# Optimization experiments

Measured on AMD Instinct MI355X. Metric: run time of the kernel, lower is better.

## Reference

```python
import jax, jax.numpy as jnp
import numpy as np

DIM = 256
HID = DIM // 8  # 32


def setup_inputs() -> dict:
    key = jax.random.key(0)
    ks = jax.random.split(key, 16)
    B, N, M, C = 4, 4096, 16, DIM
    q = jax.random.normal(ks[0], (B, N, C), dtype=jnp.float32)
    k = jax.random.normal(ks[1], (B, N, M, C), dtype=jnp.float32)
    pos = jax.random.normal(ks[2], (B, N, M, 4), dtype=jnp.float32)
    mask = jax.random.randint(ks[3], (B, N, M, 1), 0, 2, dtype=jnp.int32)
    s = 1.0 / np.sqrt(C)
    # weights stored [in, out]; apply as x @ W (+ b)
    Ws = jax.random.normal(ks[4], (C, C), dtype=jnp.float32) * s
    Wp1 = jax.random.normal(ks[5], (4, HID), dtype=jnp.float32) * 0.5
    bp1 = jnp.zeros((HID,), dtype=jnp.float32)
    Wp2 = jax.random.normal(ks[6], (HID, C), dtype=jnp.float32) * (1.0 / np.sqrt(HID))
    bp2 = jnp.zeros((C,), dtype=jnp.float32)
    Wa1 = jax.random.normal(ks[7], (C, HID), dtype=jnp.float32) * s
    ba1 = jnp.zeros((HID,), dtype=jnp.float32)
    Wa2 = jax.random.normal(ks[8], (HID, C), dtype=jnp.float32) * (1.0 / np.sqrt(HID))
    ba2 = jnp.zeros((C,), dtype=jnp.float32)
    Wo = jax.random.normal(ks[9], (C, C), dtype=jnp.float32) * s
    bo = jnp.zeros((C,), dtype=jnp.float32)
    return {"q": q, "k": k, "pos": pos, "mask": mask,
            "Ws": Ws, "Wp1": Wp1, "bp1": bp1, "Wp2": Wp2, "bp2": bp2,
            "Wa1": Wa1, "ba1": ba1, "Wa2": Wa2, "ba2": ba2,
            "Wo": Wo, "bo": bo}


def reference(q, k, pos, mask, Ws, Wp1, bp1, Wp2, bp2, Wa1, ba1, Wa2, ba2, Wo, bo):
    # shared_fc (no bias)
    q_ = q @ Ws                         # [B,N,C]
    k_ = k @ Ws                         # [B,N,M,C]
    v = k_ @ Ws                         # NOTE: source applies shared_fc twice to k
    # pos_fc: 4 -> C/8 -> C
    posf = jax.nn.relu(pos @ Wp1 + bp1) @ Wp2 + bp2   # [B,N,M,C]
    # MLP attention over (k - q + pos)
    attn = k_ - q_[:, :, None, :] + posf               # [B,N,M,C]
    attn = jax.nn.relu(attn @ Wa1 + ba1) @ Wa2 + ba2   # [B,N,M,C]
    attn = jnp.where(mask == 0, jnp.float32(-1e9), attn)
    attn = jax.nn.softmax(attn, axis=-2)               # softmax over M
    # dropout is identity in eval mode
    x = jnp.sum((v + posf) * attn, axis=2)             # [B,N,C]
    x = x @ Wo + bo
    return x
```

## Files before the change

kernel.cpp:

```cpp
#include <hip/hip_runtime.h>
#include <hip/hip_bf16.h>

typedef __attribute__((ext_vector_type(4))) float f4;
typedef __attribute__((ext_vector_type(4))) int i4;
typedef __attribute__((ext_vector_type(8))) short s8;

#define MFMA16(a,b,c) __builtin_amdgcn_mfma_f32_16x16x32_bf16((a),(b),(c),0,0,0)

static __device__ __forceinline__ unsigned short f2bf(float x){
  return __builtin_bit_cast(unsigned short, __float2bfloat16(x));
}
__device__ __forceinline__ int fidx(int kk, int c, int nct){
  return ((((kk >> 5) * nct + (c >> 4)) << 6) + (((kk >> 3) & 3) * 16 + (c & 15))) * 8 + (kk & 7);
}

__global__ void prep1(const float* __restrict__ Ws, const float* __restrict__ Wa1,
                      const float* __restrict__ Wo,
                      unsigned short* __restrict__ Ws2f, unsigned short* __restrict__ Wof,
                      unsigned short* __restrict__ WsWa1f){
  __shared__ float wrow[256];
  int i = blockIdx.x, t = threadIdx.x;
  wrow[t] = Ws[i*256 + t];
  __syncthreads();
  float a1 = 0.f;
  for (int t2 = 0; t2 < 256; ++t2) a1 += wrow[t2] * Ws[t2*256 + t];
  Ws2f[fidx(i, t, 16)] = f2bf(a1);
  Wof[fidx(i, t, 16)]  = f2bf(Wo[i*256 + t]);
  if (t < 32){
    float a2 = 0.f;
    for (int t2 = 0; t2 < 256; ++t2) a2 += wrow[t2] * Wa1[t2*32 + t];
    WsWa1f[fidx(i, t, 2)] = f2bf(a2);
  }
}

__global__ void prep2(const float* __restrict__ Wp2, const float* __restrict__ Wa2,
                      const float* __restrict__ Wa1, const float* __restrict__ bp2,
                      const float* __restrict__ ba1,
                      unsigned short* __restrict__ Wp2f, unsigned short* __restrict__ Wa2f,
                      unsigned short* __restrict__ Wp2Wa1f, float* __restrict__ bh){
  int gid = blockIdx.x * 256 + threadIdx.x;
  if (gid < 8192){
    int kk = gid >> 8, c = gid & 255;
    Wp2f[fidx(kk, c, 16)] = f2bf(Wp2[gid]);
  } else {
    int g = gid - 8192; int kk = g >> 8, c = g & 255;
    Wa2f[fidx(kk, c, 16)] = f2bf(Wa2[g]);
  }
  if (gid < 1024){
    int h1 = gid >> 5, h2 = gid & 31;
    float a = 0.f;
    for (int c = 0; c < 256; ++c) a += Wp2[h1*256 + c] * Wa1[c*32 + h2];
    Wp2Wa1f[fidx(h1, h2, 2)] = f2bf(a);
  }
  if (gid < 32){
    float a = ba1[gid];
    for (int c = 0; c < 256; ++c) a += bp2[c] * Wa1[c*32 + gid];
    bh[gid] = a;
  }
}

__global__ __attribute__((amdgpu_flat_work_group_size(256,256), amdgpu_waves_per_eu(4,4)))
void attn_x(
  const float* __restrict__ q, const float* __restrict__ k,
  const float* __restrict__ pos, const int* __restrict__ mask,
  const float* __restrict__ Wp1, const float* __restrict__ bp1,
  const float* __restrict__ bp2, const float* __restrict__ bh,
  const unsigned short* __restrict__ Ws2f, const unsigned short* __restrict__ WsWa1f,
  const unsigned short* __restrict__ Wp2f, const unsigned short* __restrict__ Wa2f,
  const unsigned short* __restrict__ Wp2Wa1f,
  unsigned short* __restrict__ xbuf)
{
  __shared__ unsigned short kA[16384];
  __shared__ unsigned short phL[2048];
  __shared__ unsigned short hL[2048];

  const int t = threadIdx.x;
  const int lane = t & 63;
  const int w = t >> 6;
  const int lg = lane >> 4;
  const int lr = lane & 15;
  const int bn0 = blockIdx.x * 4;
  const int n0 = bn0 + w;
  const f4 z4 = {0.f, 0.f, 0.f, 0.f};

  const float* krow = k + (size_t)n0 * 4096 + (size_t)lr * 256;
  const float* qrow = q + (size_t)n0 * 256;
  const unsigned short* wa1b = WsWa1f + (size_t)lane * 8;
  f4 khac[2] = {z4, z4};
  #pragma unroll
  for (int kt = 0; kt < 8; ++kt){
    int c0 = kt * 32 + lg * 8;
    f4 ka = *(const f4*)(krow + c0);
    f4 kb = *(const f4*)(krow + c0 + 4);
    f4 qa = *(const f4*)(qrow + c0);
    f4 qb = *(const f4*)(qrow + c0 + 4);
    s8 kf, mf;
    #pragma unroll
    for (int j = 0; j < 4; ++j){
      kf[j]     = (short)f2bf(ka[j]);
      kf[4 + j] = (short)f2bf(kb[j]);
      mf[j]     = (short)f2bf(ka[j] - qa[j]);
      mf[4 + j] = (short)f2bf(kb[j] - qb[j]);
    }
    *(s8*)(kA + ((w * 8 + kt) * 64 + lane) * 8) = kf;
    khac[0] = MFMA16(mf, *(const s8*)(wa1b + (size_t)(kt * 2 + 0) * 512), khac[0]);
    khac[1] = MFMA16(mf, *(const s8*)(wa1b + (size_t)(kt * 2 + 1) * 512), khac[1]);
  }

  s8 phfrag;
  {
    f4 pv = *(const f4*)(pos + (size_t)n0 * 64 + (size_t)lr * 4);
    f4 h0 = *(const f4*)(bp1 + lg * 8);
    f4 h1 = *(const f4*)(bp1 + lg * 8 + 4);
    #pragma unroll
    for (int p = 0; p < 4; ++p){
      f4 w0 = *(const f4*)(Wp1 + p * 32 + lg * 8);
      f4 w1 = *(const f4*)(Wp1 + p * 32 + lg * 8 + 4);
      #pragma unroll
      for (int j = 0; j < 4; ++j){ h0[j] += pv[p] * w0[j]; h1[j] += pv[p] * w1[j]; }
    }
    #pragma unroll
    for (int j = 0; j < 4; ++j){
      phfrag[j]     = (short)f2bf(fmaxf(h0[j], 0.f));
      phfrag[4 + j] = (short)f2bf(fmaxf(h1[j], 0.f));
    }
  }
  *(s8*)(phL + (w * 64 + lane) * 8) = phfrag;

  {
    const unsigned short* wpwb = Wp2Wa1f + (size_t)lane * 8;
    khac[0] = MFMA16(phfrag, *(const s8*)(wpwb), khac[0]);
    khac[1] = MFMA16(phfrag, *(const s8*)(wpwb + 512), khac[1]);
  }

  #pragma unroll
  for (int ct2 = 0; ct2 < 2; ++ct2){
    float bhc = bh[ct2 * 16 + lr];
    #pragma unroll
    for (int r = 0; r < 4; ++r){
      int m = lg * 4 + r, col = ct2 * 16 + lr;
      hL[w * 512 + ((col >> 3) * 16 + m) * 8 + (col & 7)] = f2bf(fmaxf(khac[ct2][r] + bhc, 0.f));
    }
  }
  __syncthreads();

  const unsigned short* ws2b = Ws2f + (size_t)lane * 8;
  const unsigned short* wp2b = Wp2f + (size_t)lane * 8;
  const unsigned short* wa2b = Wa2f + (size_t)lane * 8;

#define EPI_N(VN, N, CT, BP, BA, BP2C) { \
    s8 pfr = *(const s8*)(phL + ((N) * 64 + lane) * 8); \
    s8 hfr = *(const s8*)(hL + ((N) * 64 + lane) * 8); \
    f4 pf = MFMA16(pfr, (BP), z4); \
    f4 aa = MFMA16(hfr, (BA), z4); \
    i4 mv = *(const i4*)(mask + (size_t)(bn0 + (N)) * 16 + lg * 4); \
    float lg0 = mv[0] ? aa[0] : -1e9f; \
    float lg1 = mv[1] ? aa[1] : -1e9f; \
    float lg2 = mv[2] ? aa[2] : -1e9f; \
    float lg3 = mv[3] ? aa[3] : -1e9f; \
    float mx = fmaxf(fmaxf(lg0, lg1), fmaxf(lg2, lg3)); \
    mx = fmaxf(mx, __shfl_xor(mx, 16)); \
    mx = fmaxf(mx, __shfl_xor(mx, 32)); \
    float p0 = __expf(lg0 - mx), p1 = __expf(lg1 - mx); \
    float p2 = __expf(lg2 - mx), p3 = __expf(lg3 - mx); \
    float den = p0 + p1 + p2 + p3; \
    float num = p0 * ((VN)[0] + pf[0] + (BP2C)) \
              + p1 * ((VN)[1] + pf[1] + (BP2C)) \
              + p2 * ((VN)[2] + pf[2] + (BP2C)) \
              + p3 * ((VN)[3] + pf[3] + (BP2C)); \
    den += __shfl_xor(den, 16); den += __shfl_xor(den, 32); \
    num += __shfl_xor(num, 16); num += __shfl_xor(num, 32); \
    if (lane < 16) \
      xbuf[(size_t)(bn0 + (N)) * 256 + (CT) * 16 + lr] = f2bf(__fdividef(num, den)); \
  }

#define EPILOGUE(V0, V1, V2, V3, CT) { \
    s8 bp = *(const s8*)(wp2b + (size_t)(CT) * 512); \
    s8 ba = *(const s8*)(wa2b + (size_t)(CT) * 512); \
    float bp2c = bp2[(CT) * 16 + lr]; \
    EPI_N(V0, 0, CT, bp, ba, bp2c); \
    EPI_N(V1, 1, CT, bp, ba, bp2c); \
    EPI_N(V2, 2, CT, bp, ba, bp2c); \
    EPI_N(V3, 3, CT, bp, ba, bp2c); \
  }

  #pragma unroll
  for (int cp = 0; cp < 2; ++cp){
    const int ct0 = w * 4 + cp * 2;
    const int ct1 = ct0 + 1;
    f4 v00 = z4, v01 = z4, v02 = z4, v03 = z4;
    f4 v10 = z4, v11 = z4, v12 = z4, v13 = z4;
    #pragma unroll
    for (int kt = 0; kt < 8; ++kt){
      s8 b0 = *(const s8*)(ws2b + (size_t)(kt * 16 + ct0) * 512);
      s8 b1 = *(const s8*)(ws2b + (size_t)(kt * 16 + ct1) * 512);
      s8 af0 = *(const s8*)(kA + ((0 * 8 + kt) * 64 + lane) * 8);
      s8 af1 = *(const s8*)(kA + ((1 * 8 + kt) * 64 + lane) * 8);
      s8 af2 = *(const s8*)(kA + ((2 * 8 + kt) * 64 + lane) * 8);
      s8 af3 = *(const s8*)(kA + ((3 * 8 + kt) * 64 + lane) * 8);
      v00 = MFMA16(af0, b0, v00); v10 = MFMA16(af0, b1, v10);
      v01 = MFMA16(af1, b0, v01); v11 = MFMA16(af1, b1, v11);
      v02 = MFMA16(af2, b0, v02); v12 = MFMA16(af2, b1, v12);
      v03 = MFMA16(af3, b0, v03); v13 = MFMA16(af3, b1, v13);
    }
    EPILOGUE(v00, v01, v02, v03, ct0);
    EPILOGUE(v10, v11, v12, v13, ct1);
  }
#undef EPILOGUE
#undef EPI_N
}

__global__ __launch_bounds__(128, 4) void proj(
  const unsigned short* __restrict__ xbuf, const unsigned short* __restrict__ Wof,
  const float* __restrict__ bo, float* __restrict__ out)
{
  const int t = threadIdx.x;
  const int lane = t & 63;
  const int w = t >> 6;
  const int lg = lane >> 4;
  const int lr = lane & 15;
  const int n0 = blockIdx.x * 32 + w * 16;
  const f4 z4 = {0.f, 0.f, 0.f, 0.f};
  const unsigned short* xr = xbuf + (size_t)(n0 + lr) * 256;
  const unsigned short* wob = Wof + (size_t)lane * 8;
  #pragma unroll
  for (int p = 0; p < 4; ++p){
    f4 oac[4] = {z4, z4, z4, z4};
    #pragma unroll
    for (int kt = 0; kt < 8; ++kt){
      s8 xf = *(const s8*)(xr + kt * 32 + lg * 8);
      #pragma unroll
      for (int ci = 0; ci < 4; ++ci)
        oac[ci] = MFMA16(xf, *(const s8*)(wob + (size_t)(kt * 16 + p * 4 + ci) * 512), oac[ci]);
    }
    #pragma unroll
    for (int ci = 0; ci < 4; ++ci){
      int c = (p * 4 + ci) * 16 + lr;
      float bov = bo[c];
      #pragma unroll
      for (int r = 0; r < 4; ++r)
        out[(size_t)(n0 + lg * 4 + r) * 256 + c] = oac[ci][r] + bov;
    }
  }
}

__global__ __launch_bounds__(256, 4) void attn_mono(
  const float* __restrict__ q, const float* __restrict__ k,
  const float* __restrict__ pos, const int* __restrict__ mask,
  const float* __restrict__ Wp1, const float* __restrict__ bp1,
  const float* __restrict__ bp2, const float* __restrict__ bo,
  const float* __restrict__ bh,
  const unsigned short* __restrict__ Ws2f, const unsigned short* __restrict__ WsWa1f,
  const unsigned short* __restrict__ Wp2f, const unsigned short* __restrict__ Wa2f,
  const unsigned short* __restrict__ Wp2Wa1f, const unsigned short* __restrict__ Wof,
  float* __restrict__ out)
{
  __shared__ unsigned short kA[16384];
  __shared__ unsigned short phL[2048];
  __shared__ unsigned short hL[2048];
  __shared__ unsigned short xT[4096];

  const int t = threadIdx.x;
  const int lane = t & 63;
  const int w = t >> 6;
  const int lg = lane >> 4;
  const int lr = lane & 15;
  const int bn0 = blockIdx.x * 4;
  const int n0 = bn0 + w;
  const f4 z4 = {0.f, 0.f, 0.f, 0.f};

  const float* krow = k + (size_t)n0 * 4096 + (size_t)lr * 256;
  const float* qrow = q + (size_t)n0 * 256;
  const unsigned short* wa1b = WsWa1f + (size_t)lane * 8;
  f4 khac[2] = {z4, z4};
  #pragma unroll
  for (int kt = 0; kt < 8; ++kt){
    int c0 = kt * 32 + lg * 8;
    f4 ka = *(const f4*)(krow + c0);
    f4 kb = *(const f4*)(krow + c0 + 4);
    f4 qa = *(const f4*)(qrow + c0);
    f4 qb = *(const f4*)(qrow + c0 + 4);
    s8 kf, mf;
    #pragma unroll
    for (int j = 0; j < 4; ++j){
      kf[j]     = (short)f2bf(ka[j]);
      kf[4 + j] = (short)f2bf(kb[j]);
      mf[j]     = (short)f2bf(ka[j] - qa[j]);
      mf[4 + j] = (short)f2bf(kb[j] - qb[j]);
    }
    *(s8*)(kA + ((w * 8 + kt) * 64 + lane) * 8) = kf;
    khac[0] = MFMA16(mf, *(const s8*)(wa1b + (size_t)(kt * 2 + 0) * 512), khac[0]);
    khac[1] = MFMA16(mf, *(const s8*)(wa1b + (size_t)(kt * 2 + 1) * 512), khac[1]);
  }
  s8 phfrag;
  {
    f4 pv = *(const f4*)(pos + (size_t)n0 * 64 + (size_t)lr * 4);
    f4 h0 = *(const f4*)(bp1 + lg * 8);
    f4 h1 = *(const f4*)(bp1 + lg * 8 + 4);
    #pragma unroll
    for (int p = 0; p < 4; ++p){
      f4 w0 = *(const f4*)(Wp1 + p * 32 + lg * 8);
      f4 w1 = *(const f4*)(Wp1 + p * 32 + lg * 8 + 4);
      #pragma unroll
      for (int j = 0; j < 4; ++j){ h0[j] += pv[p] * w0[j]; h1[j] += pv[p] * w1[j]; }
    }
    #pragma unroll
    for (int j = 0; j < 4; ++j){
      phfrag[j]     = (short)f2bf(fmaxf(h0[j], 0.f));
      phfrag[4 + j] = (short)f2bf(fmaxf(h1[j], 0.f));
    }
  }
  *(s8*)(phL + (w * 64 + lane) * 8) = phfrag;
  {
    const unsigned short* wpwb = Wp2Wa1f + (size_t)lane * 8;
    khac[0] = MFMA16(phfrag, *(const s8*)(wpwb), khac[0]);
    khac[1] = MFMA16(phfrag, *(const s8*)(wpwb + 512), khac[1]);
  }
  #pragma unroll
  for (int ct2 = 0; ct2 < 2; ++ct2){
    float bhc = bh[ct2 * 16 + lr];
    #pragma unroll
    for (int r = 0; r < 4; ++r){
      int m = lg * 4 + r, col = ct2 * 16 + lr;
      hL[w * 512 + ((col >> 3) * 16 + m) * 8 + (col & 7)] = f2bf(fmaxf(khac[ct2][r] + bhc, 0.f));
    }
  }
  __syncthreads();

  const unsigned short* ws2b = Ws2f + (size_t)lane * 8;
  const unsigned short* wp2b = Wp2f + (size_t)lane * 8;
  const unsigned short* wa2b = Wa2f + (size_t)lane * 8;
  #pragma unroll
  for (int ci = 0; ci < 4; ++ci){
    int ct = w * 4 + ci;
    f4 vacc[4] = {z4, z4, z4, z4};
    #pragma unroll
    for (int kt = 0; kt < 8; ++kt){
      s8 bw = *(const s8*)(ws2b + (size_t)(kt * 16 + ct) * 512);
      #pragma unroll
      for (int n = 0; n < 4; ++n){
        s8 af = *(const s8*)(kA + ((n * 8 + kt) * 64 + lane) * 8);
        vacc[n] = MFMA16(af, bw, vacc[n]);
      }
    }
    s8 bp = *(const s8*)(wp2b + (size_t)ct * 512);
    s8 ba = *(const s8*)(wa2b + (size_t)ct * 512);
    f4 pf[4], aa[4];
    #pragma unroll
    for (int n = 0; n < 4; ++n){
      s8 pfr = *(const s8*)(phL + (n * 64 + lane) * 8);
      s8 hfr = *(const s8*)(hL + (n * 64 + lane) * 8);
      pf[n] = MFMA16(pfr, bp, z4);
      aa[n] = MFMA16(hfr, ba, z4);
    }
    float bp2c = bp2[ct * 16 + lr];
    #pragma unroll
    for (int n = 0; n < 4; ++n){
      i4 mv = *(const i4*)(mask + (size_t)(bn0 + n) * 16 + lg * 4);
      float lg0 = mv[0] ? aa[n][0] : -1e9f;
      float lg1 = mv[1] ? aa[n][1] : -1e9f;
      float lg2 = mv[2] ? aa[n][2] : -1e9f;
      float lg3 = mv[3] ? aa[n][3] : -1e9f;
      float mx = fmaxf(fmaxf(lg0, lg1), fmaxf(lg2, lg3));
      mx = fmaxf(mx, __shfl_xor(mx, 16));
      mx = fmaxf(mx, __shfl_xor(mx, 32));
      float p0 = __expf(lg0 - mx), p1 = __expf(lg1 - mx);
      float p2 = __expf(lg2 - mx), p3 = __expf(lg3 - mx);
      float den = p0 + p1 + p2 + p3;
      float num = p0 * (vacc[n][0] + pf[n][0] + bp2c)
                + p1 * (vacc[n][1] + pf[n][1] + bp2c)
                + p2 * (vacc[n][2] + pf[n][2] + bp2c)
                + p3 * (vacc[n][3] + pf[n][3] + bp2c);
      den += __shfl_xor(den, 16); den += __shfl_xor(den, 32);
      num += __shfl_xor(num, 16); num += __shfl_xor(num, 32);
      if (lane < 16){
        int c = ct * 16 + lr;
        xT[((c >> 5) * 64 + ((c >> 3) & 3) * 16 + n) * 8 + (c & 7)] = f2bf(__fdividef(num, den));
      }
    }
  }
  __syncthreads();

  f4 oac[4] = {z4, z4, z4, z4};
  const unsigned short* wob = Wof + (size_t)lane * 8;
  #pragma unroll
  for (int kt = 0; kt < 8; ++kt){
    s8 xf = *(const s8*)(xT + (kt * 64 + lane) * 8);
    #pragma unroll
    for (int ci = 0; ci < 4; ++ci)
      oac[ci] = MFMA16(xf, *(const s8*)(wob + (size_t)(kt * 16 + w * 4 + ci) * 512), oac[ci]);
  }
  if (lane < 16){
    #pragma unroll
    for (int ci = 0; ci < 4; ++ci){
      int c = (w * 4 + ci) * 16 + lr;
      float bov = bo[c];
      #pragma unroll
      for (int r = 0; r < 4; ++r)
        out[(size_t)(bn0 + r) * 256 + c] = oac[ci][r] + bov;
    }
  }
}

extern "C" void kernel_launch(void* const* d_in, const int* in_sizes, int n_in,
                              void* d_out, int out_size, void* d_ws, size_t ws_size,
                              hipStream_t stream) {
  (void)in_sizes; (void)n_in; (void)out_size;
  const float* q   = (const float*)d_in[0];
  const float* k   = (const float*)d_in[1];
  const float* pos = (const float*)d_in[2];
  const int*   msk = (const int*)d_in[3];
  const float* Ws  = (const float*)d_in[4];
  const float* Wp1 = (const float*)d_in[5];
  const float* bp1 = (const float*)d_in[6];
  const float* Wp2 = (const float*)d_in[7];
  const float* bp2 = (const float*)d_in[8];
  const float* Wa1 = (const float*)d_in[9];
  const float* ba1 = (const float*)d_in[10];
  const float* Wa2 = (const float*)d_in[11];
  const float* Wo  = (const float*)d_in[13];
  const float* bo  = (const float*)d_in[14];

  if (ws_size < 313472) return;
  char* ws = (char*)d_ws;
  unsigned short* Ws2f    = (unsigned short*)(ws + 0);
  unsigned short* Wof     = (unsigned short*)(ws + 131072);
  unsigned short* WsWa1f  = (unsigned short*)(ws + 262144);
  unsigned short* Wp2f    = (unsigned short*)(ws + 278528);
  unsigned short* Wa2f    = (unsigned short*)(ws + 294912);
  unsigned short* Wp2Wa1f = (unsigned short*)(ws + 311296);
  float*          bh      = (float*)(ws + 313344);
  unsigned short* xbuf    = (unsigned short*)(ws + 313472);

  prep1<<<dim3(256), dim3(256), 0, stream>>>(Ws, Wa1, Wo, Ws2f, Wof, WsWa1f);
  prep2<<<dim3(64), dim3(256), 0, stream>>>(Wp2, Wa2, Wa1, bp2, ba1, Wp2f, Wa2f, Wp2Wa1f, bh);

  if (ws_size >= 313472 + 8388608) {
    attn_x<<<dim3(4096), dim3(256), 0, stream>>>(q, k, pos, msk, Wp1, bp1, bp2, bh,
                                                 Ws2f, WsWa1f, Wp2f, Wa2f, Wp2Wa1f, xbuf);
    proj<<<dim3(512), dim3(128), 0, stream>>>(xbuf, Wof, bo, (float*)d_out);
  } else {
    attn_mono<<<dim3(4096), dim3(256), 0, stream>>>(q, k, pos, msk, Wp1, bp1, bp2, bo, bh,
                                                    Ws2f, WsWa1f, Wp2f, Wa2f, Wp2Wa1f, Wof,
                                                    (float*)d_out);
  }
}
```

Measured before the change: 168.1 us.

## Coalesce k loads through LDS and factor q projection out of the per-row MFMA

K rows are now loaded coalesced across the wave (each lane reads 4 contiguous floats per neighbor row), converted to bf16 and staged in LDS in fragment layout, then read back as MFMA operands. Instead of forming (k - q) per element, q is projected through WsWa1 once with separate MFMAs and subtracted from the hidden bias via a shuffle, using linearity. The aim is to cut uncoalesced global reads and VALU work. It adds LDS traffic, reuses hL as a scratch q buffer before it is written, and doubles the MFMA count in the loop, with slightly different bf16 rounding.

Measured after the change: 157.4 us. 6.4% less time.

```diff
diff --git a/kernel.cpp b/kernel.cpp
--- a/kernel.cpp
+++ b/kernel.cpp
@@ -4,6 +4,7 @@
 typedef __attribute__((ext_vector_type(4))) float f4;
 typedef __attribute__((ext_vector_type(4))) int i4;
 typedef __attribute__((ext_vector_type(8))) short s8;
+typedef __attribute__((ext_vector_type(4))) short s4;
 
 #define MFMA16(a,b,c) __builtin_amdgcn_mfma_f32_16x16x32_bf16((a),(b),(c),0,0,0)
 
@@ -83,29 +84,43 @@
   const int n0 = bn0 + w;
   const f4 z4 = {0.f, 0.f, 0.f, 0.f};
 
-  const float* krow = k + (size_t)n0 * 4096 + (size_t)lr * 256;
-  const float* qrow = q + (size_t)n0 * 256;
+  const float* kbase = k + (size_t)n0 * 4096;
+  unsigned short* kAw = kA + w * 4096;
+  unsigned short* qb  = hL + w * 512;
+  {
+    f4 qv = *(const f4*)(q + (size_t)n0 * 256 + lane * 4);
+    s4 qpk;
+    qpk[0] = (short)f2bf(qv[0]); qpk[1] = (short)f2bf(qv[1]);
+    qpk[2] = (short)f2bf(qv[2]); qpk[3] = (short)f2bf(qv[3]);
+    *(s4*)(qb + lane * 4) = qpk;
+  }
+  {
+    const int c0l = lane * 4;
+    const int kts = c0l >> 5, lgs = (c0l >> 3) & 3, js = c0l & 7;
+    unsigned short* kdst0 = kAw + ((kts * 64 + lgs * 16) << 3) + js;
+    #pragma unroll
+    for (int m = 0; m < 16; ++m){
+      f4 kv = *(const f4*)(kbase + m * 256 + c0l);
+      s4 pk;
+      pk[0] = (short)f2bf(kv[0]); pk[1] = (short)f2bf(kv[1]);
+      pk[2] = (short)f2bf(kv[2]); pk[3] = (short)f2bf(kv[3]);
+      *(s4*)(kdst0 + (m << 3)) = pk;
+    }
+  }
+
   const unsigned short* wa1b = WsWa1f + (size_t)lane * 8;
-  f4 khac[2] = {z4, z4};
+  f4 kh0 = z4, kh1 = z4, qh0 = z4, qh1 = z4;
   #pragma unroll
   for (int kt = 0; kt < 8; ++kt){
-    int c0 = kt * 32 + lg * 8;
-    f4 ka = *(const f4*)(krow + c0);
-    f4 kb = *(const f4*)(krow + c0 + 4);
-    f4 qa = *(const f4*)(qrow + c0);
-    f4 qb = *(const f4*)(qrow + c0 + 4);
-    s8 kf, mf;
-    #pragma unroll
-    for (int j = 0; j < 4; ++j){
-      kf[j]     = (short)f2bf(ka[j]);
-      kf[4 + j] = (short)f2bf(kb[j]);
-      mf[j]     = (short)f2bf(ka[j] - qa[j]);
-      mf[4 + j] = (short)f2bf(kb[j] - qb[j]);
-    }
-    *(s8*)(kA + ((w * 8 + kt) * 64 + lane) * 8) = kf;
-    khac[0] = MFMA16(mf, *(const s8*)(wa1b + (size_t)(kt * 2 + 0) * 512), khac[0]);
-    khac[1] = MFMA16(mf, *(const s8*)(wa1b + (size_t)(kt * 2 + 1) * 512), khac[1]);
-  }
+    s8 kfr = *(const s8*)(kAw + ((kt * 64 + lane) << 3));
+    s8 qfr = *(const s8*)(qb + kt * 32 + lg * 8);
+    s8 wt0 = *(const s8*)(wa1b + (size_t)(kt * 2 + 0) * 512);
+    s8 wt1 = *(const s8*)(wa1b + (size_t)(kt * 2 + 1) * 512);
+    kh0 = MFMA16(kfr, wt0, kh0);  kh1 = MFMA16(kfr, wt1, kh1);
+    qh0 = MFMA16(qfr, wt0, qh0);  qh1 = MFMA16(qfr, wt1, qh1);
+  }
+  float qhs0 = __shfl(qh0[0], lr);
+  float qhs1 = __shfl(qh1[0], lr);
 
   s8 phfrag;
   {
@@ -129,17 +144,18 @@
 
   {
     const unsigned short* wpwb = Wp2Wa1f + (size_t)lane * 8;
-    khac[0] = MFMA16(phfrag, *(const s8*)(wpwb), khac[0]);
-    khac[1] = MFMA16(phfrag, *(const s8*)(wpwb + 512), khac[1]);
+    kh0 = MFMA16(phfrag, *(const s8*)(wpwb), kh0);
+    kh1 = MFMA16(phfrag, *(const s8*)(wpwb + 512), kh1);
   }
 
   #pragma unroll
   for (int ct2 = 0; ct2 < 2; ++ct2){
-    float bhc = bh[ct2 * 16 + lr];
+    float bhc = bh[ct2 * 16 + lr] - (ct2 ? qhs1 : qhs0);
     #pragma unroll
     for (int r = 0; r < 4; ++r){
       int m = lg * 4 + r, col = ct2 * 16 + lr;
-      hL[w * 512 + ((col >> 3) * 16 + m) * 8 + (col & 7)] = f2bf(fmaxf(khac[ct2][r] + bhc, 0.f));
+      float hv = (ct2 ? kh1[r] : kh0[r]) + bhc;
+      hL[w * 512 + ((col >> 3) * 16 + m) * 8 + (col & 7)] = f2bf(fmaxf(hv, 0.f));
     }
   }
   __syncthreads();
```
